# Optimization experiments

Hardware: AMD Instinct MI355X
Metric: run time of the kernel (lower is better)

Reference implementation:

```python
import jax, jax.numpy as jnp
import numpy as np

D_NODE, C, N_HEAD = 64, 8, 8
LN_EPS = 1e-5
MASK_EPS = 1e-10
INF = 1e9


def setup_inputs() -> dict:
    key = jax.random.key(0)
    ks = jax.random.split(key, 12)
    B, S, R, D = 1, 2048, 384, D_NODE
    HC = N_HEAD * C
    M_raw = jax.random.normal(ks[0], (B, S, R, D), dtype=jnp.float32)
    M_mask = (jax.random.uniform(ks[1], (B, S, R)) > 0.1).astype(jnp.float32)
    sc = 1.0 / np.sqrt(D)
    return {
        "M_raw": M_raw,
        "M_mask": M_mask,
        "ln_g": jnp.ones((D,), jnp.float32),
        "ln_b": jnp.zeros((D,), jnp.float32),
        "Wq": jax.random.normal(ks[2], (D, HC), jnp.float32) * sc,
        "Wk": jax.random.normal(ks[3], (D, C), jnp.float32) * sc,
        "Wv": jax.random.normal(ks[4], (D, C), jnp.float32) * sc,
        "Wg": jax.random.normal(ks[5], (D, HC), jnp.float32) * sc,
        "bg": jnp.ones((HC,), jnp.float32),  # gating bias init to 1
        "Wo": jax.random.normal(ks[6], (HC, D), jnp.float32) * sc,
        "bo": jnp.zeros((D,), jnp.float32),
    }


def reference(M_raw, M_mask, ln_g, ln_b, Wq, Wk, Wv, Wg, bg, Wo, bo):
    # [B,S,R,D] -> [B,R,S,D]: attend over the sequence (column) axis per residue
    M = jnp.swapaxes(M_raw, -2, -3)
    mask = jnp.swapaxes(M_mask, -1, -2)  # [B,R,S]
    # LayerNorm over d_node
    mu = jnp.mean(M, axis=-1, keepdims=True)
    var = jnp.mean(jnp.square(M - mu), axis=-1, keepdims=True)
    M = (M - mu) * jax.lax.rsqrt(var + LN_EPS) * ln_g + ln_b
    # mean-pooled query over masked sequence positions -> [B,R,D]
    q_avg = jnp.sum(M * mask[..., None], axis=-2) / (jnp.sum(mask, axis=-1)[..., None] + MASK_EPS)
    q = (q_avg @ Wq).reshape(q_avg.shape[:-1] + (N_HEAD, C)) * (C ** -0.5)  # [B,R,H,c]
    k = M @ Wk  # [B,R,S,c] (shared across heads)
    v = M @ Wv  # [B,R,S,c]
    bias = (INF * (mask - 1.0))[..., None, :]  # [B,R,1,S]
    logits = jnp.einsum("brhc,brsc->brhs", q, k) + bias
    w = jax.nn.softmax(logits, axis=-1)
    o = jnp.einsum("brhs,brsc->brhc", w, v)  # [B,R,H,c]
    # per-position sigmoid gate broadcast against the single pooled output
    g = jax.nn.sigmoid(M @ Wg + bg).reshape(M.shape[:-1] + (N_HEAD, C))  # [B,R,S,H,c]
    go = (g * o[..., None, :, :]).reshape(M.shape[:-1] + (N_HEAD * C,))  # [B,R,S,H*c]
    out = go @ Wo + bo  # [B,R,S,D]
    return M_raw + jnp.swapaxes(out, -2, -3)
```

## Files before the change

### kernel.cpp

```cpp
#include <hip/hip_runtime.h>
#include <stdint.h>


#define DEV __device__ __forceinline__

typedef __attribute__((ext_vector_type(8))) short short8;
typedef __attribute__((ext_vector_type(4))) float floatx4;

static constexpr int S_DIM = 2048;
static constexpr int R_DIM = 384;
static constexpr int NCH   = 32;

static constexpr size_t KV_OFF    = 0;
static constexpr size_t QPART_OFF = 25165824;
static constexpr size_t O_OFF     = 28704768;

DEV float bf2f(uint32_t u) { union { uint32_t i; float f; } c; c.i = u << 16; return c.f; }
DEV uint16_t f2bf(float f) {
  union { float f; uint32_t i; } c; c.f = f;
  return (uint16_t)((c.i + 0x7FFFu + ((c.i >> 16) & 1u)) >> 16);
}
DEV void unpack8(uint4 w, float* x) {
  x[0] = bf2f(w.x & 0xffff); x[1] = bf2f(w.x >> 16);
  x[2] = bf2f(w.y & 0xffff); x[3] = bf2f(w.y >> 16);
  x[4] = bf2f(w.z & 0xffff); x[5] = bf2f(w.z >> 16);
  x[6] = bf2f(w.w & 0xffff); x[7] = bf2f(w.w >> 16);
}

__global__ __launch_bounds__(256) void k1_ln_kv(
    const float* __restrict__ M, const float* __restrict__ mask,
    const float* __restrict__ lng, const float* __restrict__ lnb,
    const float* __restrict__ Wk, const float* __restrict__ Wv,
    uint16_t* __restrict__ kv, float* __restrict__ qpart)
{
  __shared__ uint16_t WkvT[16 * 72];
  __shared__ uint16_t mlnA[4][16 * 72];
  __shared__ uint16_t kvS[4][4 * 64 * 16];

  const int tid = threadIdx.x;
  const int w = tid >> 6, lane = tid & 63;
  const int rl = lane >> 4, c4 = lane & 15;
  const int sc = blockIdx.x;
  const int s0 = sc * 64;
  const int r0w = blockIdx.y * 16 + w * 4;

#pragma unroll
  for (int i = 0; i < 4; ++i) {
    const int e = i * 256 + tid;
    const int n = e >> 6, d = e & 63;
    const float val = (n < 8) ? Wk[d * 8 + n] : Wv[d * 8 + (n - 8)];
    WkvT[n * 72 + d] = f2bf(val);
  }
  const float4 lngv = ((const float4*)lng)[c4];
  const float4 lnbv = ((const float4*)lnb)[c4];
  __syncthreads();

  const short8 b0 = *(const short8*)&WkvT[c4 * 72 + rl * 8];
  const short8 b1 = *(const short8*)&WkvT[c4 * 72 + 32 + rl * 8];

  uint16_t* mA = mlnA[w];
  uint16_t* kS = kvS[w];

  float qacc[4] = {0.f, 0.f, 0.f, 0.f};
  float cacc = 0.f;

#pragma unroll 2
  for (int grp = 0; grp < 16; ++grp) {
    const int sg = s0 + grp * 4;
    float4 xg[4];
    float mv[4];
#pragma unroll
    for (int si = 0; si < 4; ++si) {
      const size_t grow = (size_t)(sg + si) * R_DIM + r0w + rl;
      xg[si] = ((const float4*)(M + grow * 64))[c4];
      mv[si] = mask[grow];
    }
#pragma unroll
    for (int si = 0; si < 4; ++si) {
      const float4 x = xg[si];
      float sum = x.x + x.y + x.z + x.w;
      float ss = x.x * x.x + x.y * x.y + x.z * x.z + x.w * x.w;
#pragma unroll
      for (int off = 1; off < 16; off <<= 1) {
        sum += __shfl_xor(sum, off, 64);
        ss  += __shfl_xor(ss, off, 64);
      }
      const float mu = sum * (1.f / 64.f);
      const float var = ss * (1.f / 64.f) - mu * mu;
      const float rstd = 1.f / sqrtf(var + 1e-5f);
      float y[4];
      y[0] = (x.x - mu) * rstd * lngv.x + lnbv.x;
      y[1] = (x.y - mu) * rstd * lngv.y + lnbv.y;
      y[2] = (x.z - mu) * rstd * lngv.z + lnbv.z;
      y[3] = (x.w - mu) * rstd * lngv.w + lnbv.w;
      uint2 p;
      p.x = (uint32_t)f2bf(y[0]) | ((uint32_t)f2bf(y[1]) << 16);
      p.y = (uint32_t)f2bf(y[2]) | ((uint32_t)f2bf(y[3]) << 16);
      *(uint2*)&mA[(si * 4 + rl) * 72 + c4 * 4] = p;
      const float m = mv[si];
      qacc[0] += m * y[0]; qacc[1] += m * y[1];
      qacc[2] += m * y[2]; qacc[3] += m * y[3];
      cacc += m;
    }
    const short8 a0 = *(const short8*)&mA[c4 * 72 + rl * 8];
    const short8 a1 = *(const short8*)&mA[c4 * 72 + 32 + rl * 8];
    floatx4 c = {0.f, 0.f, 0.f, 0.f};
    c = __builtin_amdgcn_mfma_f32_16x16x32_bf16(a0, b0, c, 0, 0, 0);
    c = __builtin_amdgcn_mfma_f32_16x16x32_bf16(a1, b1, c, 0, 0, 0);
#pragma unroll
    for (int i = 0; i < 4; ++i)
      kS[i * 1024 + (grp * 4 + rl) * 16 + c4] = f2bf(c[i]);
  }

#pragma unroll
  for (int i = 0; i < 4; ++i) {
#pragma unroll
    for (int t = 0; t < 2; ++t) {
      const uint4 val = *(const uint4*)&kS[i * 1024 + t * 512 + lane * 8];
      *(uint4*)(kv + ((size_t)(r0w + i) * S_DIM + s0) * 16 + t * 512 + lane * 8) = val;
    }
  }
  *(float4*)&qpart[((size_t)(r0w + rl) * NCH + sc) * 72 + c4 * 4] =
      make_float4(qacc[0], qacc[1], qacc[2], qacc[3]);
  if (c4 == 0)
    qpart[((size_t)(r0w + rl) * NCH + sc) * 72 + 64] = cacc;
}

__global__ __launch_bounds__(256) void k2_attn(
    const float* __restrict__ Wq, const float* __restrict__ mask,
    const uint16_t* __restrict__ kv, const float* __restrict__ qpart,
    float* __restrict__ oG)
{
  __shared__ float qavgL[64], qLs[64];
  __shared__ float redmax[4][8], redden[4][8], redo[4][64];
  __shared__ float cntL;
  const int tid = threadIdx.x;
  const int r = blockIdx.x;
  const int lane = tid & 63, wv = tid >> 6;

  float qs = 0.f;
  if (tid < 65) {
#pragma unroll
    for (int c = 0; c < NCH; ++c) qs += qpart[((size_t)r * NCH + c) * 72 + tid];
    if (tid == 64) cntL = qs;
  }
  __syncthreads();
  if (tid < 64) qavgL[tid] = qs / (cntL + 1e-10f);
  __syncthreads();
  if (tid < 64) {
    float a = 0.f;
    for (int d = 0; d < 64; ++d) a += qavgL[d] * Wq[d * 64 + tid];
    qLs[tid] = a * 0.35355339059327373f;
  }
  __syncthreads();

  float l[64];
  float lm[8];
#pragma unroll
  for (int h = 0; h < 8; ++h) lm[h] = -3.0e38f;
  const uint4* kvp = (const uint4*)kv;
#pragma unroll
  for (int it = 0; it < 8; ++it) {
    const int s = it * 256 + tid;
    uint4 kw = kvp[((size_t)r * S_DIM + s) * 2];
    float k[8]; unpack8(kw, k);
    const float bias = (mask[(size_t)s * R_DIM + r] - 1.f) * 1e9f;
#pragma unroll
    for (int h = 0; h < 8; ++h) {
      float t = bias;
#pragma unroll
      for (int c = 0; c < 8; ++c) t += qLs[h * 8 + c] * k[c];
      l[it * 8 + h] = t;
      lm[h] = fmaxf(lm[h], t);
    }
  }
#pragma unroll
  for (int h = 0; h < 8; ++h)
#pragma unroll
    for (int off = 1; off < 64; off <<= 1) lm[h] = fmaxf(lm[h], __shfl_xor(lm[h], off, 64));
  if (lane == 0) {
#pragma unroll
    for (int h = 0; h < 8; ++h) redmax[wv][h] = lm[h];
  }
  __syncthreads();
  float gm[8];
#pragma unroll
  for (int h = 0; h < 8; ++h)
    gm[h] = fmaxf(fmaxf(redmax[0][h], redmax[1][h]), fmaxf(redmax[2][h], redmax[3][h]));

  float den[8], ao[64];
#pragma unroll
  for (int h = 0; h < 8; ++h) den[h] = 0.f;
#pragma unroll
  for (int i = 0; i < 64; ++i) ao[i] = 0.f;
#pragma unroll
  for (int it = 0; it < 8; ++it) {
    const int s = it * 256 + tid;
    uint4 vw = kvp[((size_t)r * S_DIM + s) * 2 + 1];
    float v[8]; unpack8(vw, v);
#pragma unroll
    for (int h = 0; h < 8; ++h) {
      const float w = __expf(l[it * 8 + h] - gm[h]);
      den[h] += w;
#pragma unroll
      for (int c = 0; c < 8; ++c) ao[h * 8 + c] += w * v[c];
    }
  }
#pragma unroll
  for (int st = 5; st >= 0; --st) {
    const int dist = 1 << st;
    const bool hi = (lane & dist) != 0;
#pragma unroll
    for (int j = 0; j < (1 << st); ++j) {
      const float send = hi ? ao[j] : ao[j + dist];
      const float recv = __shfl_xor(send, dist, 64);
      ao[j] = (hi ? ao[j + dist] : ao[j]) + recv;
    }
  }
#pragma unroll
  for (int h = 0; h < 8; ++h)
#pragma unroll
    for (int off = 1; off < 64; off <<= 1) den[h] += __shfl_xor(den[h], off, 64);

  redo[wv][lane] = ao[0];
  if (lane == 0) {
#pragma unroll
    for (int h = 0; h < 8; ++h) redden[wv][h] = den[h];
  }
  __syncthreads();
  if (tid < 64) {
    const float o = redo[0][tid] + redo[1][tid] + redo[2][tid] + redo[3][tid];
    const int h = tid >> 3;
    const float dd = redden[0][h] + redden[1][h] + redden[2][h] + redden[3][h];
    oG[(size_t)r * 64 + tid] = o / dd;
  }
}

__global__ __launch_bounds__(256, 2) void k3_out(
    const float* __restrict__ M, const float* __restrict__ oG,
    const float* __restrict__ Wg, const float* __restrict__ bg,
    const float* __restrict__ Wo, const float* __restrict__ bo,
    const float* __restrict__ lng, const float* __restrict__ lnb,
    float* __restrict__ out)
{
  __shared__ uint16_t WgT[64 * 72];
  __shared__ uint16_t WoT[64 * 72];
  __shared__ uint16_t mlnA[4][16 * 72];
  __shared__ uint16_t tA[4][16 * 72];

  const int tid = threadIdx.x;
  const int w = tid >> 6, lane = tid & 63;
  const int rl = lane >> 4, c4 = lane & 15;
  const int sc = blockIdx.x;
  const int s0 = sc * 64;
  const int r0w = blockIdx.y * 16 + w * 4;

#pragma unroll
  for (int i = 0; i < 16; ++i) {
    const int idx = i * 256 + tid;
    const int a = idx >> 6, b = idx & 63;
    WgT[b * 72 + a] = f2bf(Wg[idx]);
    WoT[b * 72 + a] = f2bf(Wo[idx]);
  }
  const float4 lngv = ((const float4*)lng)[c4];
  const float4 lnbv = ((const float4*)lnb)[c4];
  __syncthreads();

  short8 wgB[4][2], woB[4][2];
#pragma unroll
  for (int nt = 0; nt < 4; ++nt)
#pragma unroll
    for (int kk = 0; kk < 2; ++kk) {
      wgB[nt][kk] = *(const short8*)&WgT[(nt * 16 + c4) * 72 + kk * 32 + rl * 8];
      woB[nt][kk] = *(const short8*)&WoT[(nt * 16 + c4) * 72 + kk * 32 + rl * 8];
    }
  float og[4][4], bgr[4], bor[4];
#pragma unroll
  for (int nt = 0; nt < 4; ++nt) {
    bgr[nt] = bg[nt * 16 + c4];
    bor[nt] = bo[nt * 16 + c4];
#pragma unroll
    for (int i = 0; i < 4; ++i)
      og[nt][i] = oG[(size_t)(r0w + i) * 64 + nt * 16 + c4];
  }

  uint16_t* mA = mlnA[w];
  uint16_t* tAw = tA[w];

#pragma unroll 2
  for (int grp = 0; grp < 16; ++grp) {
    const int sg = s0 + grp * 4;
    float4 xg[4];
#pragma unroll
    for (int si = 0; si < 4; ++si)
      xg[si] = ((const float4*)(M + ((size_t)(sg + si) * R_DIM + r0w + rl) * 64))[c4];

#pragma unroll
    for (int si = 0; si < 4; ++si) {
      const float4 x = xg[si];
      float sum = x.x + x.y + x.z + x.w;
      float ss = x.x * x.x + x.y * x.y + x.z * x.z + x.w * x.w;
#pragma unroll
      for (int off = 1; off < 16; off <<= 1) {
        sum += __shfl_xor(sum, off, 64);
        ss  += __shfl_xor(ss, off, 64);
      }
      const float mu = sum * (1.f / 64.f);
      const float var = ss * (1.f / 64.f) - mu * mu;
      const float rstd = 1.f / sqrtf(var + 1e-5f);
      float y[4];
      y[0] = (x.x - mu) * rstd * lngv.x + lnbv.x;
      y[1] = (x.y - mu) * rstd * lngv.y + lnbv.y;
      y[2] = (x.z - mu) * rstd * lngv.z + lnbv.z;
      y[3] = (x.w - mu) * rstd * lngv.w + lnbv.w;
      uint2 p;
      p.x = (uint32_t)f2bf(y[0]) | ((uint32_t)f2bf(y[1]) << 16);
      p.y = (uint32_t)f2bf(y[2]) | ((uint32_t)f2bf(y[3]) << 16);
      *(uint2*)&mA[(si * 4 + rl) * 72 + c4 * 4] = p;
    }

    {
      const short8 a0 = *(const short8*)&mA[c4 * 72 + rl * 8];
      const short8 a1 = *(const short8*)&mA[c4 * 72 + 32 + rl * 8];
#pragma unroll
      for (int nt = 0; nt < 4; ++nt) {
        floatx4 c = {0.f, 0.f, 0.f, 0.f};
        c = __builtin_amdgcn_mfma_f32_16x16x32_bf16(a0, wgB[nt][0], c, 0, 0, 0);
        c = __builtin_amdgcn_mfma_f32_16x16x32_bf16(a1, wgB[nt][1], c, 0, 0, 0);
#pragma unroll
        for (int i = 0; i < 4; ++i) {
          const float z = c[i] + bgr[nt];
          const float gt = 1.0f / (1.0f + __expf(-z));
          tAw[(rl * 4 + i) * 72 + nt * 16 + c4] = f2bf(gt * og[nt][i]);
        }
      }
    }
    {
      const short8 a0 = *(const short8*)&tAw[c4 * 72 + rl * 8];
      const short8 a1 = *(const short8*)&tAw[c4 * 72 + 32 + rl * 8];
#pragma unroll
      for (int nt = 0; nt < 4; ++nt) {
        floatx4 c = {0.f, 0.f, 0.f, 0.f};
        c = __builtin_amdgcn_mfma_f32_16x16x32_bf16(a0, woB[nt][0], c, 0, 0, 0);
        c = __builtin_amdgcn_mfma_f32_16x16x32_bf16(a1, woB[nt][1], c, 0, 0, 0);
#pragma unroll
        for (int i = 0; i < 4; ++i)
          mA[(rl * 4 + i) * 72 + nt * 16 + c4] = f2bf(c[i] + bor[nt]);
      }
    }
#pragma unroll
    for (int si = 0; si < 4; ++si) {
      const uint2 tv = *(const uint2*)&mA[(si * 4 + rl) * 72 + c4 * 4];
      const float4 x = xg[si];
      float4 o;
      o.x = x.x + bf2f(tv.x & 0xffff);
      o.y = x.y + bf2f(tv.x >> 16);
      o.z = x.z + bf2f(tv.y & 0xffff);
      o.w = x.w + bf2f(tv.y >> 16);
      ((float4*)(out + ((size_t)(sg + si) * R_DIM + r0w + rl) * 64))[c4] = o;
    }
  }
}

extern "C" void kernel_launch(void* const* d_in, const int* in_sizes, int n_in,
                              void* d_out, int out_size, void* d_ws, size_t ws_size,
                              hipStream_t stream)
{
  const float* M    = (const float*)d_in[0];
  const float* mask = (const float*)d_in[1];
  const float* lng  = (const float*)d_in[2];
  const float* lnb  = (const float*)d_in[3];
  const float* Wq   = (const float*)d_in[4];
  const float* Wk   = (const float*)d_in[5];
  const float* Wv   = (const float*)d_in[6];
  const float* Wg   = (const float*)d_in[7];
  const float* bg   = (const float*)d_in[8];
  const float* Wo   = (const float*)d_in[9];
  const float* bo   = (const float*)d_in[10];
  float* out = (float*)d_out;

  char* ws = (char*)d_ws;
  uint16_t* kvB  = (uint16_t*)(ws + KV_OFF);
  float* qpartB  = (float*)(ws + QPART_OFF);
  float* oB      = (float*)(ws + O_OFF);

  k1_ln_kv<<<dim3(NCH, 24), 256, 0, stream>>>(M, mask, lng, lnb, Wk, Wv, kvB, qpartB);
  k2_attn<<<dim3(R_DIM), 256, 0, stream>>>(Wq, mask, kvB, qpartB, oB);
  k3_out<<<dim3(NCH, 24), 256, 0, stream>>>(M, oB, Wg, bg, Wo, bo, lng, lnb, out);
}
```

Baseline: 457.6 us.

## Prefetch next row group, shrink kv staging, use packed bf16 converts, raise occupancy

```diff
diff --git a/kernel.cpp b/kernel.cpp
--- a/kernel.cpp
+++ b/kernel.cpp
@@ -1,4 +1,5 @@
 #include <hip/hip_runtime.h>
+#include <hip/hip_bf16.h>
 #include <stdint.h>
 
 
@@ -16,9 +17,13 @@
 static constexpr size_t O_OFF     = 28704768;
 
 DEV float bf2f(uint32_t u) { union { uint32_t i; float f; } c; c.i = u << 16; return c.f; }
-DEV uint16_t f2bf(float f) {
-  union { float f; uint32_t i; } c; c.f = f;
-  return (uint16_t)((c.i + 0x7FFFu + ((c.i >> 16) & 1u)) >> 16);
+DEV uint32_t pk2bf(float lo, float hi) {
+  __hip_bfloat162 h2 = __float22bfloat162_rn(make_float2(lo, hi));
+  union { __hip_bfloat162 h; uint32_t u; } cv; cv.h = h2; return cv.u;
+}
+DEV uint16_t f2bf_hw(float f) {
+  __hip_bfloat16 h = __float2bfloat16(f);
+  union { __hip_bfloat16 h; uint16_t u; } cv; cv.h = h; return cv.u;
 }
 DEV void unpack8(uint4 w, float* x) {
   x[0] = bf2f(w.x & 0xffff); x[1] = bf2f(w.x >> 16);
@@ -27,7 +32,7 @@
   x[6] = bf2f(w.w & 0xffff); x[7] = bf2f(w.w >> 16);
 }
 
-__global__ __launch_bounds__(256) void k1_ln_kv(
+__global__ __launch_bounds__(256, 4) void k1_ln_kv(
     const float* __restrict__ M, const float* __restrict__ mask,
     const float* __restrict__ lng, const float* __restrict__ lnb,
     const float* __restrict__ Wk, const float* __restrict__ Wv,
@@ -35,7 +40,7 @@
 {
   __shared__ uint16_t WkvT[16 * 72];
   __shared__ uint16_t mlnA[4][16 * 72];
-  __shared__ uint16_t kvS[4][4 * 64 * 16];
+  __shared__ uint16_t kvS[4][1024];
 
   const int tid = threadIdx.x;
   const int w = tid >> 6, lane = tid & 63;
@@ -49,7 +54,7 @@
     const int e = i * 256 + tid;
     const int n = e >> 6, d = e & 63;
     const float val = (n < 8) ? Wk[d * 8 + n] : Wv[d * 8 + (n - 8)];
-    WkvT[n * 72 + d] = f2bf(val);
+    WkvT[n * 72 + d] = f2bf_hw(val);
   }
   const float4 lngv = ((const float4*)lng)[c4];
   const float4 lnbv = ((const float4*)lnb)[c4];
@@ -64,17 +69,27 @@
   float qacc[4] = {0.f, 0.f, 0.f, 0.f};
   float cacc = 0.f;
 
+  float4 xg[4];
+  float mv[4];
+#pragma unroll
+  for (int si = 0; si < 4; ++si) {
+    const size_t grow = (size_t)(s0 + si) * R_DIM + r0w + rl;
+    xg[si] = ((const float4*)(M + grow * 64))[c4];
+    mv[si] = mask[grow];
+  }
+
 #pragma unroll 2
   for (int grp = 0; grp < 16; ++grp) {
-    const int sg = s0 + grp * 4;
-    float4 xg[4];
-    float mv[4];
+    const int gn = (grp < 15) ? grp + 1 : 15;
+    float4 xn[4];
+    float mn[4];
 #pragma unroll
     for (int si = 0; si < 4; ++si) {
-      const size_t grow = (size_t)(sg + si) * R_DIM + r0w + rl;
-      xg[si] = ((const float4*)(M + grow * 64))[c4];
-      mv[si] = mask[grow];
-    }
+      const size_t grow = (size_t)(s0 + gn * 4 + si) * R_DIM + r0w + rl;
+      xn[si] = ((const float4*)(M + grow * 64))[c4];
+      mn[si] = mask[grow];
+    }
+
 #pragma unroll
     for (int si = 0; si < 4; ++si) {
       const float4 x = xg[si];
@@ -94,8 +109,8 @@
       y[2] = (x.z - mu) * rstd * lngv.z + lnbv.z;
       y[3] = (x.w - mu) * rstd * lngv.w + lnbv.w;
       uint2 p;
-      p.x = (uint32_t)f2bf(y[0]) | ((uint32_t)f2bf(y[1]) << 16);
-      p.y = (uint32_t)f2bf(y[2]) | ((uint32_t)f2bf(y[3]) << 16);
+      p.x = pk2bf(y[0], y[1]);
+      p.y = pk2bf(y[2], y[3]);
       *(uint2*)&mA[(si * 4 + rl) * 72 + c4 * 4] = p;
       const float m = mv[si];
       qacc[0] += m * y[0]; qacc[1] += m * y[1];
@@ -109,17 +124,21 @@
     c = __builtin_amdgcn_mfma_f32_16x16x32_bf16(a1, b1, c, 0, 0, 0);
 #pragma unroll
     for (int i = 0; i < 4; ++i)
-      kS[i * 1024 + (grp * 4 + rl) * 16 + c4] = f2bf(c[i]);
-  }
-
-#pragma unroll
-  for (int i = 0; i < 4; ++i) {
-#pragma unroll
-    for (int t = 0; t < 2; ++t) {
-      const uint4 val = *(const uint4*)&kS[i * 1024 + t * 512 + lane * 8];
-      *(uint4*)(kv + ((size_t)(r0w + i) * S_DIM + s0) * 16 + t * 512 + lane * 8) = val;
-    }
-  }
+      kS[i * 256 + ((grp & 3) * 4 + rl) * 16 + c4] = f2bf_hw(c[i]);
+
+    if ((grp & 3) == 3) {
+      const int sb = grp >> 2;
+      const int rI = lane >> 4, li = lane & 15;
+#pragma unroll
+      for (int t = 0; t < 4; ++t) {
+        const uint2 val = *(const uint2*)&kS[rI * 256 + t * 64 + li * 4];
+        *(uint2*)(kv + ((size_t)(r0w + rI) * S_DIM + s0 + sb * 16) * 16 + t * 64 + li * 4) = val;
+      }
+    }
+#pragma unroll
+    for (int si = 0; si < 4; ++si) { xg[si] = xn[si]; mv[si] = mn[si]; }
+  }
+
   *(float4*)&qpart[((size_t)(r0w + rl) * NCH + sc) * 72 + c4 * 4] =
       make_float4(qacc[0], qacc[1], qacc[2], qacc[3]);
   if (c4 == 0)
@@ -236,7 +255,7 @@
   }
 }
 
-__global__ __launch_bounds__(256, 2) void k3_out(
+__global__ __launch_bounds__(256, 3) void k3_out(
     const float* __restrict__ M, const float* __restrict__ oG,
     const float* __restrict__ Wg, const float* __restrict__ bg,
     const float* __restrict__ Wo, const float* __restrict__ bo,
@@ -259,8 +278,8 @@
   for (int i = 0; i < 16; ++i) {
     const int idx = i * 256 + tid;
     const int a = idx >> 6, b = idx & 63;
-    WgT[b * 72 + a] = f2bf(Wg[idx]);
-    WoT[b * 72 + a] = f2bf(Wo[idx]);
+    WgT[b * 72 + a] = f2bf_hw(Wg[idx]);
+    WoT[b * 72 + a] = f2bf_hw(Wo[idx]);
   }
   const float4 lngv = ((const float4*)lng)[c4];
   const float4 lnbv = ((const float4*)lnb)[c4];
@@ -314,8 +333,8 @@
       y[2] = (x.z - mu) * rstd * lngv.z + lnbv.z;
       y[3] = (x.w - mu) * rstd * lngv.w + lnbv.w;
       uint2 p;
-      p.x = (uint32_t)f2bf(y[0]) | ((uint32_t)f2bf(y[1]) << 16);
-      p.y = (uint32_t)f2bf(y[2]) | ((uint32_t)f2bf(y[3]) << 16);
+      p.x = pk2bf(y[0], y[1]);
+      p.y = pk2bf(y[2], y[3]);
       *(uint2*)&mA[(si * 4 + rl) * 72 + c4 * 4] = p;
     }
 
@@ -331,7 +350,7 @@
         for (int i = 0; i < 4; ++i) {
           const float z = c[i] + bgr[nt];
           const float gt = 1.0f / (1.0f + __expf(-z));
-          tAw[(rl * 4 + i) * 72 + nt * 16 + c4] = f2bf(gt * og[nt][i]);
+          tAw[(rl * 4 + i) * 72 + nt * 16 + c4] = f2bf_hw(gt * og[nt][i]);
         }
       }
     }
@@ -345,7 +364,7 @@
         c = __builtin_amdgcn_mfma_f32_16x16x32_bf16(a1, woB[nt][1], c, 0, 0, 0);
 #pragma unroll
         for (int i = 0; i < 4; ++i)
-          mA[(rl * 4 + i) * 72 + nt * 16 + c4] = f2bf(c[i] + bor[nt]);
+          mA[(rl * 4 + i) * 72 + nt * 16 + c4] = f2bf_hw(c[i] + bor[nt]);
       }
     }
 #pragma unroll
```

Result: no change. 453.4 us (-0.9%).
